# Kernel optimization log

Hardware: AMD Instinct MI355X
Metric: run time of the kernel (lower is better)

The kernel has to match this reference:

```python
import jax, jax.numpy as jnp
import numpy as np

B, T, D, H = 2, 2048, 1024, 16
DH = D // H
PD = 6
SCALE = DH ** -0.5
_PAIRS4 = [(0, 1), (0, 2), (0, 3), (1, 2), (1, 3), (2, 3)]
_J6 = jnp.array([[0, 0, 0, 0, 0, 1], [0, 0, 0, 0, -1, 0], [0, 0, 0, 1, 0, 0],
                 [0, 0, 1, 0, 0, 0], [0, -1, 0, 0, 0, 0], [1, 0, 0, 0, 0, 0]], dtype=jnp.float32)


def exterior(p1, p2):
    # p1, p2: (..., 4) -> normalized 6-d Plucker line (..., 6)
    parts = [p1[..., i] * p2[..., j] - p1[..., j] * p2[..., i] for i, j in _PAIRS4]
    L = jnp.stack(parts, axis=-1)
    n = jnp.linalg.norm(L, axis=-1, keepdims=True)
    return L / jnp.clip(n, 1e-12)


def setup_inputs() -> dict:
    key = jax.random.key(0)
    ks = jax.random.split(key, 12)
    s = 0.02
    return {
        'x': jax.random.normal(ks[0], (B, T, D), jnp.float32),
        'qkv_w': jax.random.normal(ks[1], (D, 3 * D), jnp.float32) * s,
        'qkv_b': jnp.zeros((3 * D,), jnp.float32),
        'w1_write': jax.random.normal(ks[2], (D, 4 * H), jnp.float32) * s,
        'w2_write': jax.random.normal(ks[3], (D, 4 * H), jnp.float32) * s,
        'w1_read': jax.random.normal(ks[4], (D, 4 * H), jnp.float32) * s,
        'w2_read': jax.random.normal(ks[5], (D, 4 * H), jnp.float32) * s,
        'memv_w': jax.random.normal(ks[6], (D, D), jnp.float32) * s,
        'memv_b': jnp.zeros((D,), jnp.float32),
        'memg_w': jax.random.normal(ks[7], (D, H), jnp.float32) * s,
        'memg_b': jnp.zeros((H,), jnp.float32),
        'mem_scale': jnp.full((H,), 0.1, jnp.float32),
        'rw_mix': jnp.zeros((), jnp.float32),
        'out_w': jax.random.normal(ks[8], (D, D), jnp.float32) * s,
        'out_b': jnp.zeros((D,), jnp.float32),
        'decay_logits': jnp.full((H,), 4.6, jnp.float32),
    }


def reference(x, qkv_w, qkv_b, w1_write, w2_write, w1_read, w2_read,
              memv_w, memv_b, memg_w, memg_b, mem_scale, rw_mix,
              out_w, out_b, decay_logits):
    # ---- standard causal softmax attention ----
    qkv = (x @ qkv_w + qkv_b).reshape(B, T, 3, H, DH).transpose(2, 0, 3, 1, 4)
    q, k, v = qkv[0], qkv[1], qkv[2]                      # each (B,H,T,DH)
    scores = jnp.einsum('bhtd,bhsd->bhts', q, k) * SCALE
    mask = jnp.triu(jnp.ones((T, T), bool), 1)
    scores = jnp.where(mask[None, None], -jnp.inf, scores)
    attn = jax.nn.softmax(scores, axis=-1)                # dropout=0 (eval)
    seq_out = jnp.einsum('bhts,bhsd->bthd', attn, v).reshape(B, T, D)

    # ---- Plucker lines for write (prev->cur) and read ----
    x_prev = jnp.concatenate([jnp.zeros((B, 1, D), x.dtype), x[:, :-1]], axis=1)
    w1 = (x_prev @ w1_write).reshape(B, T, H, 4)
    w2 = (x @ w2_write).reshape(B, T, H, 4)
    write_lines = exterior(w1, w2)                        # (B,T,H,6)
    r1 = (x @ w1_read).reshape(B, T, H, 4)
    r2 = (x @ w2_read).reshape(B, T, H, 4)
    read_lines = exterior(r1, r2)

    Jw = jnp.einsum('bthi,ij->bhtj', write_lines, _J6)    # (B,H,T,6)
    Jr = jnp.einsum('bthi,ij->bhtj', read_lines, _J6)
    rd = read_lines.transpose(0, 2, 1, 3)                 # (B,H,T,6)

    # ---- decay-weighted cumsum of 6x6 outer-product states ----
    decays = jax.nn.sigmoid(decay_logits)                 # (H,)
    pos = jnp.arange(T, dtype=x.dtype)
    decay_inv = (1.0 / jnp.clip(decays, 1e-6))[:, None] ** pos[None]   # (H,T)
    decay_fwd = decays[:, None] ** pos[None]                           # (H,T)

    def shifted_state(Jv):
        outer = Jv[..., :, None] * Jv[..., None, :]       # (B,H,T,6,6)
        ow = outer * decay_inv[None, :, :, None, None]
        M = jnp.cumsum(ow, axis=2)
        M = jnp.concatenate([jnp.zeros((B, H, 1, PD, PD), x.dtype), M[:, :, :-1]], axis=2)
        return M * decay_fwd[None, :, :, None, None]

    Mw = shifted_state(Jw)
    Mr = shifted_state(Jr)

    score_w = jnp.einsum('bhti,bhtij,bhtj->bht', rd, Mw, rd)
    score_r = jnp.einsum('bhti,bhtij,bhtj->bht', Jw, Mr, Jw)
    alpha = jax.nn.sigmoid(rw_mix)
    mem_score = (1 - alpha) * score_w + alpha * score_r   # (B,H,T)

    mem_val = x @ memv_w + memv_b                         # (B,T,D)
    gate = jax.nn.sigmoid(x @ memg_w + memg_b)            # (B,T,H)
    mem_score_t = mem_score.transpose(0, 2, 1)            # (B,T,H)
    gated = jax.nn.sigmoid(mem_score_t * mem_scale[None, None, :]) * gate
    gated = gated.mean(axis=-1, keepdims=True)            # (B,T,1)

    return (seq_out + gated * mem_val) @ out_w + out_b
```

## Files before the change

### kernel.cpp

```cpp
#include <hip/hip_runtime.h>

#define Bb 2
#define Tt 2048
#define Dd 1024
#define Hh 16
#define LDC 4480

typedef __attribute__((ext_vector_type(8))) short s16x8;
typedef __attribute__((ext_vector_type(4))) float f32x4;
typedef __attribute__((ext_vector_type(8))) _Float16 f16x8;

__device__ __forceinline__ float bf2f(unsigned short u) {
  unsigned v = ((unsigned)u) << 16;
  union { unsigned u; float f; } c; c.u = v; return c.f;
}
__device__ __forceinline__ unsigned short f2bf(float f) {
  union { float f; unsigned u; } c; c.f = f;
  unsigned u = c.u + 0x7fffu + ((c.u >> 16) & 1u);
  return (unsigned short)(u >> 16);
}
__device__ __forceinline__ float sigm(float x) { return 1.f / (1.f + expf(-x)); }

typedef const __attribute__((address_space(1))) void* gas_ptr;
typedef __attribute__((address_space(3))) void* las_ptr;
__device__ __forceinline__ void gload_lds16(const unsigned short* g, unsigned short* l) {
  __builtin_amdgcn_global_load_lds((gas_ptr)g, (las_ptr)l, 16, 0, 0);
}



__global__ __launch_bounds__(256) void prep_kernel(const float* __restrict__ x,
                                                   const float* __restrict__ qkv_w,
                                                   const float* __restrict__ w1w,
                                                   const float* __restrict__ w2w,
                                                   const float* __restrict__ w1r,
                                                   const float* __restrict__ w2r,
                                                   const float* __restrict__ memg_w,
                                                   const float* __restrict__ memv_w,
                                                   const float* __restrict__ out_w,
                                                   const float* __restrict__ qkv_b,
                                                   const float* __restrict__ memg_b,
                                                   const float* __restrict__ memv_b,
                                                   unsigned short* __restrict__ xb,
                                                   unsigned short* __restrict__ WT,
                                                   unsigned short* __restrict__ outT,
                                                   float* __restrict__ biasC) {
  __shared__ float tile[32][33];
  int id = blockIdx.x;
  if (id < 2048) {
    int i = id * 256 + threadIdx.x;
    int row = i >> 7;
    int k8 = i & 127;
    const float4* xv = reinterpret_cast<const float4*>(x + (size_t)i * 8);
    float4 a = xv[0], b = xv[1];
    s16x8 out;
    out[0] = (short)f2bf(a.x); out[1] = (short)f2bf(a.y);
    out[2] = (short)f2bf(a.z); out[3] = (short)f2bf(a.w);
    out[4] = (short)f2bf(b.x); out[5] = (short)f2bf(b.y);
    out[6] = (short)f2bf(b.z); out[7] = (short)f2bf(b.w);
    int mt = row >> 4, kt = k8 >> 2, quad = k8 & 3;
    int lane = (row & 15) + quad * 16;
    *(s16x8*)&xb[(((size_t)mt * 32 + kt) * 64 + lane) * 8] = out;
  } else if (id < 6528) {
    int j = id - 2048;
    int n0 = (j % 140) * 32, kt = j / 140, k0 = kt * 32;
    int tx = threadIdx.x & 31, ty = threadIdx.x >> 5;
#pragma unroll
    for (int i = 0; i < 4; i++) {
      int k = k0 + ty + i * 8, n = n0 + tx;
      float v;
      if (n < 3072)       v = qkv_w[(size_t)k * 3072 + n];
      else if (n < 3136)  v = w1w[k * 64 + (n - 3072)];
      else if (n < 3200)  v = w2w[k * 64 + (n - 3136)];
      else if (n < 3264)  v = w1r[k * 64 + (n - 3200)];
      else if (n < 3328)  v = w2r[k * 64 + (n - 3264)];
      else if (n < 3344)  v = memg_w[k * 16 + (n - 3328)];
      else if (n < 3392)  v = 0.f;
      else if (n < 4416)  v = memv_w[(size_t)k * 1024 + (n - 3392)];
      else                v = 0.f;
      tile[ty + i * 8][tx] = v;
    }
    __syncthreads();
    if (threadIdx.x < 128) {
      int nl = threadIdx.x & 31, quad = threadIdx.x >> 5;
      s16x8 out;
#pragma unroll
      for (int e = 0; e < 8; e++) out[e] = (short)f2bf(tile[quad * 8 + e][nl]);
      int nt = (n0 >> 4) + (nl >> 4);
      int lane = (nl & 15) + quad * 16;
      *(s16x8*)&WT[(((size_t)nt * 32 + kt) * 64 + lane) * 8] = out;
    }
  } else if (id < 7552) {
    int j = id - 6528;
    int n0 = (j & 31) * 32, kt = j >> 5, k0 = kt * 32;
    int tx = threadIdx.x & 31, ty = threadIdx.x >> 5;
#pragma unroll
    for (int i = 0; i < 4; i++) {
      int k = k0 + ty + i * 8, n = n0 + tx;
      tile[ty + i * 8][tx] = out_w[(size_t)k * 1024 + n];
    }
    __syncthreads();
    if (threadIdx.x < 128) {
      int nl = threadIdx.x & 31, quad = threadIdx.x >> 5;
      s16x8 out;
#pragma unroll
      for (int e = 0; e < 8; e++) out[e] = (short)f2bf(tile[quad * 8 + e][nl]);
      int nt = (n0 >> 4) + (nl >> 4);
      int lane = (nl & 15) + quad * 16;
      *(s16x8*)&outT[(((size_t)nt * 32 + kt) * 64 + lane) * 8] = out;
    }
  } else {
    int i = (id - 7552) * 256 + threadIdx.x;
    if (i < LDC) {
      float v = 0.f;
      if (i < 3072) v = qkv_b[i];
      else if (i >= 3328 && i < 3344) v = memg_b[i - 3328];
      else if (i >= 3392 && i < 4416) v = memv_b[i - 3392];
      biasC[i] = v;
    }
  }
}


__global__ __launch_bounds__(256, 2) void gemm_fat_kernel(const unsigned short* __restrict__ Af,
                                                          const unsigned short* __restrict__ Bf,
                                                          unsigned short* __restrict__ Cout,
                                                          const float* __restrict__ bias) {
  const int blk = blockIdx.x;
  const int xcd = blk & 7, local = blk >> 3;
  const int mTile = (xcd & 3) * 8 + (local & 7);
  const int nTile = (xcd >> 2) * 9 + (local >> 3);
  const int lane = threadIdx.x & 63, wid = threadIdx.x >> 6;
  const int quad = lane >> 4, c16 = lane & 15;
  const int wm = wid & 1, wn = wid >> 1;
  const int mt0 = mTile * 8 + wm * 4;
  const int nt0 = nTile * 16 + wn * 8;

  const unsigned short* Apt = Af + ((size_t)mt0 * 32 * 64 + lane) * 8;
  const unsigned short* Bpt = Bf + ((size_t)nt0 * 32 * 64 + lane) * 8;

  f32x4 acc[4][8] = {};
  s16x8 af[2][4];
  s16x8 bf[2][8];
#pragma unroll
  for (int i = 0; i < 4; i++) af[0][i] = *(const s16x8*)(Apt + (size_t)i * 16384);
#pragma unroll
  for (int j = 0; j < 8; j++) bf[0][j] = *(const s16x8*)(Bpt + (size_t)j * 16384);

#pragma unroll
  for (int kt = 0; kt < 32; kt++) {
    const int cur = kt & 1, nxt = cur ^ 1;
    if (kt + 1 < 32) {
      const unsigned short* An = Apt + (size_t)(kt + 1) * 512;
      const unsigned short* Bn = Bpt + (size_t)(kt + 1) * 512;
#pragma unroll
      for (int i = 0; i < 4; i++) af[nxt][i] = *(const s16x8*)(An + (size_t)i * 16384);
#pragma unroll
      for (int j = 0; j < 8; j++) bf[nxt][j] = *(const s16x8*)(Bn + (size_t)j * 16384);
    }
#pragma unroll
    for (int i = 0; i < 4; i++)
#pragma unroll
      for (int j = 0; j < 8; j++)
        acc[i][j] = __builtin_amdgcn_mfma_f32_16x16x32_bf16(af[cur][i], bf[cur][j],
                                                            acc[i][j], 0, 0, 0);
  }

#pragma unroll
  for (int i = 0; i < 4; i++)
#pragma unroll
    for (int j = 0; j < 8; j++) {
      if (nt0 + j < 280) {
        int col = (nt0 + j) * 16 + c16;
        float bv = bias[col];
#pragma unroll
        for (int r = 0; r < 4; r++) {
          int row = (mt0 + i) * 16 + quad * 4 + r;
          Cout[(size_t)row * 4480 + col] = f2bf(acc[i][j][r] + bv);
        }
      }
    }
}


template <int MODE>
__global__ __launch_bounds__(256) void gemm_frag_kernel(const unsigned short* __restrict__ Af,
                                                        const unsigned short* __restrict__ Bf,
                                                        void* __restrict__ Cout,
                                                        const float* __restrict__ bias) {
  __shared__ __align__(16) unsigned short lds[2][16][512];
  int mTile, nTile;
  if (MODE == 0) {
    const int xx = blockIdx.x & 7, local = blockIdx.x >> 3;
    mTile = (xx >> 1) * 8 + (local & 7);
    nTile = (xx & 1) * 18 + (local >> 3);
    if (nTile >= 35) return;
  } else {
    mTile = blockIdx.x >> 3;
    nTile = blockIdx.x & 7;
  }
  const int lane = threadIdx.x & 63, wid = threadIdx.x >> 6;
  const int quad = lane >> 4, c16 = lane & 15;
  const int wm = wid >> 1, wn = wid & 1;
  const int mt0 = mTile * 8 + wm * 4;
  const int nt0 = nTile * 8 + wn * 4;

  const unsigned short* src[4];
#pragma unroll
  for (int i = 0; i < 4; i++) {
    int f = wid * 4 + i;
    src[i] = ((f < 8) ? (Af + (size_t)(mTile * 8 + f) * 16384)
                      : (Bf + (size_t)(nTile * 8 + (f - 8)) * 16384))
             + (size_t)lane * 8;
  }

  f32x4 acc[4][4] = {};

#pragma unroll
  for (int i = 0; i < 4; i++) gload_lds16(src[i], &lds[0][wid * 4 + i][0]);
  __syncthreads();

  int buf = 0;
  for (int kt = 0; kt < 32; kt++) {
    if (kt + 1 < 32) {
#pragma unroll
      for (int i = 0; i < 4; i++)
        gload_lds16(src[i] + (size_t)(kt + 1) * 512, &lds[buf ^ 1][wid * 4 + i][0]);
    }
    s16x8 a[4], b[4];
#pragma unroll
    for (int i = 0; i < 4; i++) {
      a[i] = *(const s16x8*)&lds[buf][wm * 4 + i][lane * 8];
      b[i] = *(const s16x8*)&lds[buf][8 + wn * 4 + i][lane * 8];
    }
#pragma unroll
    for (int mt = 0; mt < 4; mt++)
#pragma unroll
      for (int nt = 0; nt < 4; nt++)
        acc[mt][nt] = __builtin_amdgcn_mfma_f32_16x16x32_bf16(a[mt], b[nt],
                                                              acc[mt][nt], 0, 0, 0);
    __syncthreads();
    buf ^= 1;
  }

#pragma unroll
  for (int mt = 0; mt < 4; mt++)
#pragma unroll
    for (int nt = 0; nt < 4; nt++) {
      int col = (nt0 + nt) * 16 + c16;
      float bv = bias[col];
#pragma unroll
      for (int r = 0; r < 4; r++) {
        int row = (mt0 + mt) * 16 + quad * 4 + r;
        if (MODE == 0)
          ((unsigned short*)Cout)[(size_t)row * 4480 + col] = f2bf(acc[mt][nt][r] + bv);
        else
          ((float*)Cout)[(size_t)row * 1024 + col] = acc[mt][nt][r] + bv;
      }
    }
}


__device__ __forceinline__ void ext6(const float* p, const float* q, float* L) {
  L[0] = p[0] * q[1] - p[1] * q[0];
  L[1] = p[0] * q[2] - p[2] * q[0];
  L[2] = p[0] * q[3] - p[3] * q[0];
  L[3] = p[1] * q[2] - p[2] * q[1];
  L[4] = p[1] * q[3] - p[3] * q[1];
  L[5] = p[2] * q[3] - p[3] * q[2];
  float n = sqrtf(L[0]*L[0] + L[1]*L[1] + L[2]*L[2] + L[3]*L[3] + L[4]*L[4] + L[5]*L[5]);
  float inv = 1.f / fmaxf(n, 1e-12f);
#pragma unroll
  for (int k = 0; k < 6; k++) L[k] *= inv;
}


__global__ __launch_bounds__(256) void post1_kernel(const unsigned short* __restrict__ Cq,
                                                    unsigned short* __restrict__ Kt,
                                                    unsigned short* __restrict__ Vt,
                                                    float* __restrict__ Jw,
                                                    float* __restrict__ Jr,
                                                    float* __restrict__ rd) {
  __shared__ unsigned short vt[32 * 66];
  int id = blockIdx.x;
  int tid = threadIdx.x;
  if (id < 2048) {
    int kb = id & 63, bh = id >> 6;
    int b = bh >> 4, h = bh & 15;
    size_t tbase = ((size_t)bh * 64 + kb) * 2048;
    {
      int key = tid >> 3, p = tid & 7, dg = p ^ (key & 7);
      size_t src = (size_t)(b * Tt + kb * 32 + key) * LDC + 1024 + h * 64 + dg * 8;
      s16x8 kv = *(const s16x8*)&Cq[src];
      s16x8 kvs;
#pragma unroll
      for (int e = 0; e < 8; e++)
        kvs[e] = (short)f2bf(bf2f((unsigned short)kv[e]) * 0.125f);
      *(s16x8*)&Kt[tbase + (size_t)tid * 8] = kvs;
    }
    {
      int row = tid >> 3, c = tid & 7;
      size_t src = (size_t)(b * Tt + kb * 32 + row) * LDC + 2048 + h * 64 + c * 8;
      s16x8 vv = *(const s16x8*)&Cq[src];
#pragma unroll
      for (int e = 0; e < 8; e++) {
        union { _Float16 hf; unsigned short s; } cv;
        cv.hf = (_Float16)bf2f((unsigned short)vv[e]);
        vt[row * 66 + c * 8 + e] = cv.s;
      }
    }
    __syncthreads();
    {
      int d = tid >> 2, p = tid & 3, cq = p ^ ((d >> 2) & 3);
      s16x8 out;
#pragma unroll
      for (int e = 0; e < 8; e++) {
        int key = ((e >> 2) & 1) * 16 + cq * 4 + (e & 3);
        out[e] = (short)vt[key * 66 + d];
      }
      *(s16x8*)&Vt[tbase + (size_t)tid * 8] = out;
    }
  } else {
    int idx = (id - 2048) * 256 + tid;
    int h = idx & 15, t = (idx >> 4) & 2047, b = idx >> 15;
    size_t row = (size_t)(b * Tt + t) * LDC;
    float w1[4], w2[4], r1[4], r2[4];
#pragma unroll
    for (int k = 0; k < 4; k++) {
      w1[k] = (t > 0) ? bf2f(Cq[row - LDC + 3072 + h * 4 + k]) : 0.f;
      w2[k] = bf2f(Cq[row + 3136 + h * 4 + k]);
      r1[k] = bf2f(Cq[row + 3200 + h * 4 + k]);
      r2[k] = bf2f(Cq[row + 3264 + h * 4 + k]);
    }
    float Lw[6], Lr[6];
    ext6(w1, w2, Lw);
    ext6(r1, r2, Lr);
    size_t ob = ((size_t)(b * Hh + h) * Tt + t) * 6;
    Jw[ob + 0] = Lw[5]; Jw[ob + 1] = -Lw[4]; Jw[ob + 2] = Lw[3];
    Jw[ob + 3] = Lw[2]; Jw[ob + 4] = -Lw[1]; Jw[ob + 5] = Lw[0];
    Jr[ob + 0] = Lr[5]; Jr[ob + 1] = -Lr[4]; Jr[ob + 2] = Lr[3];
    Jr[ob + 3] = Lr[2]; Jr[ob + 4] = -Lr[1]; Jr[ob + 5] = Lr[0];
#pragma unroll
    for (int k = 0; k < 6; k++) rd[ob + k] = Lr[k];
  }
}


__device__ __forceinline__ void do_tile(int ks, int q0, int quad, int c16,
                                        const s16x8& qf0, const s16x8& qf1,
                                        const s16x8 kf[2][2], const f16x8 vb[4],
                                        float& l_i, f32x4 o[4]) {
  f32x4 st0 = {}, st1 = {};
  __builtin_amdgcn_s_setprio(1);
  st0 = __builtin_amdgcn_mfma_f32_16x16x32_bf16(kf[0][0], qf0, st0, 0, 0, 0);
  st0 = __builtin_amdgcn_mfma_f32_16x16x32_bf16(kf[0][1], qf1, st0, 0, 0, 0);
  st1 = __builtin_amdgcn_mfma_f32_16x16x32_bf16(kf[1][0], qf0, st1, 0, 0, 0);
  st1 = __builtin_amdgcn_mfma_f32_16x16x32_bf16(kf[1][1], qf1, st1, 0, 0, 0);
  __builtin_amdgcn_s_setprio(0);
  bool need_mask = (ks + 31 > q0);
  f16x8 pa;
  float lp = 0.f;
#pragma unroll
  for (int r = 0; r < 4; r++) {
    float v0 = st0[r];
    float v1 = st1[r];
    if (need_mask) {
      v0 = (ks + quad * 4 + r      <= q0 + c16) ? v0 : -1e30f;
      v1 = (ks + 16 + quad * 4 + r <= q0 + c16) ? v1 : -1e30f;
    }
    float p0 = __expf(v0);
    float p1 = __expf(v1);
    lp += p0 + p1;
    pa[r]     = (_Float16)p0;
    pa[4 + r] = (_Float16)p1;
  }
  l_i += lp;
  __builtin_amdgcn_s_setprio(1);
#pragma unroll
  for (int nt = 0; nt < 4; nt++)
    o[nt] = __builtin_amdgcn_mfma_f32_16x16x32_f16(pa, vb[nt], o[nt], 0, 0, 0);
  __builtin_amdgcn_s_setprio(0);
}

__global__ __launch_bounds__(128, 2) void attn_kernel(const unsigned short* __restrict__ Cq,
                                                      const unsigned short* __restrict__ Kt,
                                                      const unsigned short* __restrict__ Vt,
                                                      unsigned short* __restrict__ po) {
  __shared__ float mrg[64][69];
  const int id = blockIdx.x;
  const int xcd = id & 7, rest = id >> 3;
  const int j = rest & 31;
  const int bh = ((rest >> 5) << 3) | xcd;
  const int b = bh >> 4, h = bh & 15;
  const int kw = threadIdx.x >> 6, lane = threadIdx.x & 63;
  const int quad = lane >> 4, c16 = lane & 15;
  const int qA0r = j * 32,        qA1r = j * 32 + 16;
  const int qB0r = 2016 - j * 32, qB1r = 2032 - j * 32;
  const int Ttot = 64 - j;
  const int ht = (j >= 16) ? 16 : (32 - j);
  const int t0 = kw ? ht : 0;
  const int t1 = kw ? Ttot : ht;
  const char* Kbase = (const char*)(Kt + (size_t)bh * 64 * 2048);
  const char* Vbase = (const char*)(Vt + (size_t)bh * 64 * 2048);
  const int vK0 = c16 * 128 + ((quad       ^ (c16 & 7)) * 16);
  const int vK1 = c16 * 128 + (((4 + quad) ^ (c16 & 7)) * 16);
  const int vV  = c16 * 64  + ((quad ^ ((c16 >> 2) & 3)) * 16);

  size_t rowA0 = (size_t)(b * Tt + qA0r + c16) * LDC + h * 64;
  size_t rowA1 = (size_t)(b * Tt + qA1r + c16) * LDC + h * 64;
  size_t rowB0 = (size_t)(b * Tt + qB0r + c16) * LDC + h * 64;
  size_t rowB1 = (size_t)(b * Tt + qB1r + c16) * LDC + h * 64;
  s16x8 qa00 = *(const s16x8*)&Cq[rowA0 + quad * 8];
  s16x8 qa01 = *(const s16x8*)&Cq[rowA0 + 32 + quad * 8];
  s16x8 qa10 = *(const s16x8*)&Cq[rowA1 + quad * 8];
  s16x8 qa11 = *(const s16x8*)&Cq[rowA1 + 32 + quad * 8];
  s16x8 qb00 = *(const s16x8*)&Cq[rowB0 + quad * 8];
  s16x8 qb01 = *(const s16x8*)&Cq[rowB0 + 32 + quad * 8];
  s16x8 qb10 = *(const s16x8*)&Cq[rowB1 + quad * 8];
  s16x8 qb11 = *(const s16x8*)&Cq[rowB1 + 32 + quad * 8];

  float lA0 = 0.f, lA1 = 0.f, lB0 = 0.f, lB1 = 0.f;
  f32x4 oA0[4] = {}, oA1[4] = {}, oB0[4] = {}, oB1[4] = {};

  s16x8 kfX[2][2], kfY[2][2];
  f16x8 vbX[4], vbY[4];

#define LOADT(dstK, dstV, kb) do {                                   \
    const char* Kb_ = Kbase + (size_t)(kb) * 4096;                   \
    const char* Vb_ = Vbase + (size_t)(kb) * 4096;                   \
    dstK[0][0] = *(const s16x8*)(Kb_ + vK0);                         \
    dstK[0][1] = *(const s16x8*)(Kb_ + vK1);                         \
    dstK[1][0] = *(const s16x8*)(Kb_ + 2048 + vK0);                  \
    dstK[1][1] = *(const s16x8*)(Kb_ + 2048 + vK1);                  \
    dstV[0] = *(const f16x8*)(Vb_ + vV);                             \
    dstV[1] = *(const f16x8*)(Vb_ + 1024 + vV);                      \
    dstV[2] = *(const f16x8*)(Vb_ + 2048 + vV);                      \
    dstV[3] = *(const f16x8*)(Vb_ + 3072 + vV);                      \
  } while (0)

#define DOTILES(KF, VF, t) do {                                      \
    int ks_ = (t) * 32;                                              \
    do_tile(ks_, qB0r, quad, c16, qb00, qb01, KF, VF, lB0, oB0);     \
    do_tile(ks_, qB1r, quad, c16, qb10, qb11, KF, VF, lB1, oB1);     \
    if ((t) <= j) {                                                  \
      do_tile(ks_, qA0r, quad, c16, qa00, qa01, KF, VF, lA0, oA0);   \
      do_tile(ks_, qA1r, quad, c16, qa10, qa11, KF, VF, lA1, oA1);   \
    }                                                                \
  } while (0)

  LOADT(kfX, vbX, t0);
  for (int t = t0; t < t1; t += 2) {
    if (t + 1 < t1) LOADT(kfY, vbY, t + 1);
    DOTILES(kfX, vbX, t);
    if (t + 1 < t1) {
      if (t + 2 < t1) LOADT(kfX, vbX, t + 2);
      DOTILES(kfY, vbY, t + 1);
    }
  }
#undef DOTILES
#undef LOADT

  if (kw == 1) {
#pragma unroll
    for (int nt = 0; nt < 4; nt++)
#pragma unroll
      for (int r = 0; r < 4; r++) {
        mrg[lane][nt * 4 + r]      = oB0[nt][r];
        mrg[lane][16 + nt * 4 + r] = oB1[nt][r];
        mrg[lane][32 + nt * 4 + r] = oA0[nt][r];
        mrg[lane][48 + nt * 4 + r] = oA1[nt][r];
      }
    mrg[lane][64] = lB0;
    mrg[lane][65] = lB1;
    mrg[lane][66] = lA0;
    mrg[lane][67] = lA1;
  }
  __syncthreads();
  if (kw == 1) return;
#pragma unroll
  for (int nt = 0; nt < 4; nt++)
#pragma unroll
    for (int r = 0; r < 4; r++) {
      oB0[nt][r] += mrg[lane][nt * 4 + r];
      oB1[nt][r] += mrg[lane][16 + nt * 4 + r];
      oA0[nt][r] += mrg[lane][32 + nt * 4 + r];
      oA1[nt][r] += mrg[lane][48 + nt * 4 + r];
    }
  lB0 += mrg[lane][64];
  lB1 += mrg[lane][65];
  lA0 += mrg[lane][66];
  lA1 += mrg[lane][67];

  lB0 += __shfl_xor(lB0, 16, 64); lB0 += __shfl_xor(lB0, 32, 64);
  lB1 += __shfl_xor(lB1, 16, 64); lB1 += __shfl_xor(lB1, 32, 64);
  lA0 += __shfl_xor(lA0, 16, 64); lA0 += __shfl_xor(lA0, 32, 64);
  lA1 += __shfl_xor(lA1, 16, 64); lA1 += __shfl_xor(lA1, 32, 64);
  float invB0 = 1.f / lB0, invB1 = 1.f / lB1;
  float invA0 = 1.f / lA0, invA1 = 1.f / lA1;
#pragma unroll
  for (int r = 0; r < 4; r++) {
    float ivB0 = __shfl(invB0, quad * 4 + r, 64);
    float ivB1 = __shfl(invB1, quad * 4 + r, 64);
    float ivA0 = __shfl(invA0, quad * 4 + r, 64);
    float ivA1 = __shfl(invA1, quad * 4 + r, 64);
    size_t bB0 = (size_t)(b * Tt + qB0r + quad * 4 + r) * Dd + h * 64;
    size_t bB1 = (size_t)(b * Tt + qB1r + quad * 4 + r) * Dd + h * 64;
    size_t bA0 = (size_t)(b * Tt + qA0r + quad * 4 + r) * Dd + h * 64;
    size_t bA1 = (size_t)(b * Tt + qA1r + quad * 4 + r) * Dd + h * 64;
#pragma unroll
    for (int nt = 0; nt < 4; nt++) {
      po[bB0 + nt * 16 + c16] = f2bf(oB0[nt][r] * ivB0);
      po[bB1 + nt * 16 + c16] = f2bf(oB1[nt][r] * ivB1);
      po[bA0 + nt * 16 + c16] = f2bf(oA0[nt][r] * ivA0);
      po[bA1 + nt * 16 + c16] = f2bf(oA1[nt][r] * ivA1);
    }
  }
}


__global__ __launch_bounds__(64) void scanA_kernel(const float* __restrict__ Jw,
                                                   const float* __restrict__ Jr,
                                                   const float* __restrict__ decay_logits,
                                                   float* __restrict__ chunkA) {
  int blk = blockIdx.x;
  int chunk = blk & 15, bh = (blk >> 4) & 31, type = blk >> 9;
  int lane = threadIdx.x;
  const float* V = (type == 0 ? Jw : Jr) + ((size_t)bh * Tt + chunk * 128) * 6;
  __shared__ float v[768];
  for (int i = lane; i < 768; i += 64) v[i] = V[i];
  __syncthreads();
  float d = sigm(decay_logits[bh & 15]);
  int ll = lane < 36 ? lane : 35;
  int i6 = ll / 6, j6 = ll % 6;
  float A = 0.f;
  for (int s = 0; s < 128; s++) A = d * A + v[s * 6 + i6] * v[s * 6 + j6];
  if (lane < 36) chunkA[((size_t)(type * 32 + bh) * 16 + chunk) * 36 + lane] = A;
}


__global__ __launch_bounds__(128) void scanB_kernel(const float* __restrict__ Jw,
                                                    const float* __restrict__ Jr,
                                                    const float* __restrict__ rd,
                                                    const float* __restrict__ chunkA,
                                                    const float* __restrict__ decay_logits,
                                                    float* __restrict__ score_w,
                                                    float* __restrict__ score_r) {
  int blk = blockIdx.x;
  int chunk = blk & 15, bh = (blk >> 4) & 31, type = blk >> 9;
  int tl = threadIdx.x;
  size_t tb = ((size_t)bh * Tt + chunk * 128) * 6;
  const float* U = (type == 0 ? rd : Jw) + tb;
  const float* W = (type == 0 ? Jw : Jr) + tb;
  __shared__ float wv[768];
  __shared__ float Bm[36];
  for (int i = tl; i < 768; i += 128) wv[i] = W[i];
  float d = sigm(decay_logits[bh & 15]);
  if (tl < 36) {
    float dS = powf(d, 128.f);
    float Bv = 0.f;
    size_t base = (size_t)(type * 32 + bh) * 16;
    for (int c = 0; c < chunk; c++)
      Bv = dS * Bv + d * chunkA[(base + c) * 36 + tl];
    Bm[tl] = Bv;
  }
  __syncthreads();
  float u[6];
#pragma unroll
  for (int i = 0; i < 6; i++) u[i] = U[tl * 6 + i];
  float q = 0.f;
#pragma unroll
  for (int i = 0; i < 6; i++) {
    float bi = 0.f;
#pragma unroll
    for (int j = 0; j < 6; j++) bi += Bm[i * 6 + j] * u[j];
    q += u[i] * bi;
  }
  float acc = 0.f;
  for (int s = 0; s < tl; s++) {
    const float* ws = &wv[s * 6];
    float dot = u[0]*ws[0] + u[1]*ws[1] + u[2]*ws[2] + u[3]*ws[3] + u[4]*ws[4] + u[5]*ws[5];
    acc = d * (acc + dot * dot);
  }
  float score = acc + powf(d, (float)tl) * q;
  float* outp = (type == 0 ? score_w : score_r);
  outp[(size_t)bh * Tt + chunk * 128 + tl] = score;
}


__global__ __launch_bounds__(256) void combine_kernel(const unsigned short* __restrict__ po,
                                                      const unsigned short* __restrict__ Cq,
                                                      const float* __restrict__ score_w,
                                                      const float* __restrict__ score_r,
                                                      const float* __restrict__ mem_scale,
                                                      const float* __restrict__ rw_mix,
                                                      unsigned short* __restrict__ fused) {
  __shared__ float tmp[16];
  int rowi = blockIdx.x;
  int b = rowi >> 11, t = rowi & 2047;
  float alpha = sigm(rw_mix[0]);
  if (threadIdx.x < 16) {
    int h = threadIdx.x;
    size_t sh = (size_t)(b * 16 + h) * Tt + t;
    float ms = (1.f - alpha) * score_w[sh] + alpha * score_r[sh];
    float gate = sigm(bf2f(Cq[(size_t)rowi * LDC + 3328 + h]));
    tmp[h] = sigm(ms * mem_scale[h]) * gate;
  }
  __syncthreads();
  float g = 0.f;
#pragma unroll
  for (int h = 0; h < 16; h++) g += tmp[h];
  g *= (1.f / 16.f);
  if (threadIdx.x < 128) {
    int c = threadIdx.x;
    int d0 = c * 8;
    s16x8 ov = *(const s16x8*)&po[((size_t)b * Tt + t) * Dd + d0];
    s16x8 mv = *(const s16x8*)&Cq[(size_t)rowi * LDC + 3392 + d0];
    s16x8 out;
#pragma unroll
    for (int e = 0; e < 8; e++)
      out[e] = (short)f2bf(bf2f((unsigned short)ov[e]) + g * bf2f((unsigned short)mv[e]));
    int mt = rowi >> 4, kt = c >> 2, quad = c & 3;
    int lane = (rowi & 15) + quad * 16;
    *(s16x8*)&fused[(((size_t)mt * 32 + kt) * 64 + lane) * 8] = out;
  }
}


extern "C" void kernel_launch(void* const* d_in, const int* in_sizes, int n_in,
                              void* d_out, int out_size, void* d_ws, size_t ws_size,
                              hipStream_t stream) {
  (void)in_sizes; (void)n_in; (void)out_size; (void)ws_size;
  const float* x         = (const float*)d_in[0];
  const float* qkv_w     = (const float*)d_in[1];
  const float* qkv_b     = (const float*)d_in[2];
  const float* w1w       = (const float*)d_in[3];
  const float* w2w       = (const float*)d_in[4];
  const float* w1r       = (const float*)d_in[5];
  const float* w2r       = (const float*)d_in[6];
  const float* memv_w    = (const float*)d_in[7];
  const float* memv_b    = (const float*)d_in[8];
  const float* memg_w    = (const float*)d_in[9];
  const float* memg_b    = (const float*)d_in[10];
  const float* mem_scale = (const float*)d_in[11];
  const float* rw_mix    = (const float*)d_in[12];
  const float* out_w     = (const float*)d_in[13];
  const float* out_b     = (const float*)d_in[14];
  const float* decay_l   = (const float*)d_in[15];

  char* w = (char*)d_ws;
  unsigned short* xb    = (unsigned short*)(w + 0);
  unsigned short* Kt    = (unsigned short*)(w + 0);
  unsigned short* WT    = (unsigned short*)(w + 8388608);
  unsigned short* Vt    = (unsigned short*)(w + 8388608);
  unsigned short* outT  = (unsigned short*)(w + 17563648);
  float*          biasC = (float*)(w + 19660800);
  unsigned short* Cbuf  = (unsigned short*)(w + 19678720);
  unsigned short* po    = (unsigned short*)(w + 56378880);
  float*          Jw    = (float*)(w + 73680384);
  float*          Jr    = (float*)(w + 75253248);
  float*          rd    = (float*)(w + 76826112);
  float*          chA   = (float*)(w + 78398976);
  float*          sw    = (float*)(w + 78693888);
  float*          sr    = (float*)(w + 78956032);
  unsigned short* fused = (unsigned short*)(w + 79218176);

  prep_kernel<<<7570, 256, 0, stream>>>(x, qkv_w, w1w, w2w, w1r, w2r, memg_w, memv_w,
                                        out_w, qkv_b, memg_b, memv_b,
                                        xb, WT, outT, biasC);

  gemm_fat_kernel<<<576, 256, 0, stream>>>(xb, WT, Cbuf, biasC);

  post1_kernel<<<2304, 256, 0, stream>>>(Cbuf, Kt, Vt, Jw, Jr, rd);
  attn_kernel<<<1024, 128, 0, stream>>>(Cbuf, Kt, Vt, po);
  scanA_kernel<<<1024, 64, 0, stream>>>(Jw, Jr, decay_l, chA);
  scanB_kernel<<<1024, 128, 0, stream>>>(Jw, Jr, rd, chA, decay_l, sw, sr);
  combine_kernel<<<4096, 256, 0, stream>>>(po, Cbuf, sw, sr, mem_scale, rw_mix, fused);

  gemm_frag_kernel<1><<<256, 256, 0, stream>>>(fused, outT, d_out, out_b);
}
```

Baseline: 305.4 us.

## Rebalance prep, QKV GEMM, combine and output GEMM grids

The weight-transpose prep blocks now each handle four k-tiles, which cuts the prep grid to fewer blocks. The register-fed fat QKV GEMM is replaced by the LDS-staged frag GEMM in mode 0. The combine kernel now processes two rows per block so all 256 threads do work. A new output GEMM with 128x64 tiles launches 512 blocks instead of 256 for better CU occupancy. Each change trades per-block work against launch overhead and parallelism, and the swapped QKV GEMM path may behave differently in performance.

```diff
diff --git a/kernel.cpp b/kernel.cpp
--- a/kernel.cpp
+++ b/kernel.cpp
@@ -61,56 +61,64 @@
     int mt = row >> 4, kt = k8 >> 2, quad = k8 & 3;
     int lane = (row & 15) + quad * 16;
     *(s16x8*)&xb[(((size_t)mt * 32 + kt) * 64 + lane) * 8] = out;
-  } else if (id < 6528) {
+  } else if (id < 3168) {
     int j = id - 2048;
-    int n0 = (j % 140) * 32, kt = j / 140, k0 = kt * 32;
+    int n0 = (j % 140) * 32, kt0 = (j / 140) * 4;
     int tx = threadIdx.x & 31, ty = threadIdx.x >> 5;
-#pragma unroll
-    for (int i = 0; i < 4; i++) {
-      int k = k0 + ty + i * 8, n = n0 + tx;
-      float v;
-      if (n < 3072)       v = qkv_w[(size_t)k * 3072 + n];
-      else if (n < 3136)  v = w1w[k * 64 + (n - 3072)];
-      else if (n < 3200)  v = w2w[k * 64 + (n - 3136)];
-      else if (n < 3264)  v = w1r[k * 64 + (n - 3200)];
-      else if (n < 3328)  v = w2r[k * 64 + (n - 3264)];
-      else if (n < 3344)  v = memg_w[k * 16 + (n - 3328)];
-      else if (n < 3392)  v = 0.f;
-      else if (n < 4416)  v = memv_w[(size_t)k * 1024 + (n - 3392)];
-      else                v = 0.f;
-      tile[ty + i * 8][tx] = v;
-    }
-    __syncthreads();
-    if (threadIdx.x < 128) {
-      int nl = threadIdx.x & 31, quad = threadIdx.x >> 5;
-      s16x8 out;
-#pragma unroll
-      for (int e = 0; e < 8; e++) out[e] = (short)f2bf(tile[quad * 8 + e][nl]);
-      int nt = (n0 >> 4) + (nl >> 4);
-      int lane = (nl & 15) + quad * 16;
-      *(s16x8*)&WT[(((size_t)nt * 32 + kt) * 64 + lane) * 8] = out;
-    }
-  } else if (id < 7552) {
-    int j = id - 6528;
-    int n0 = (j & 31) * 32, kt = j >> 5, k0 = kt * 32;
+    for (int kk = 0; kk < 4; kk++) {
+      int kt = kt0 + kk, k0 = kt * 32;
+#pragma unroll
+      for (int i = 0; i < 4; i++) {
+        int k = k0 + ty + i * 8, n = n0 + tx;
+        float v;
+        if (n < 3072)       v = qkv_w[(size_t)k * 3072 + n];
+        else if (n < 3136)  v = w1w[k * 64 + (n - 3072)];
+        else if (n < 3200)  v = w2w[k * 64 + (n - 3136)];
+        else if (n < 3264)  v = w1r[k * 64 + (n - 3200)];
+        else if (n < 3328)  v = w2r[k * 64 + (n - 3264)];
+        else if (n < 3344)  v = memg_w[k * 16 + (n - 3328)];
+        else if (n < 3392)  v = 0.f;
+        else if (n < 4416)  v = memv_w[(size_t)k * 1024 + (n - 3392)];
+        else                v = 0.f;
+        tile[ty + i * 8][tx] = v;
+      }
+      __syncthreads();
+      if (threadIdx.x < 128) {
+        int nl = threadIdx.x & 31, quad = threadIdx.x >> 5;
+        s16x8 out;
+#pragma unroll
+        for (int e = 0; e < 8; e++) out[e] = (short)f2bf(tile[quad * 8 + e][nl]);
+        int nt = (n0 >> 4) + (nl >> 4);
+        int lane = (nl & 15) + quad * 16;
+        *(s16x8*)&WT[(((size_t)nt * 32 + kt) * 64 + lane) * 8] = out;
+      }
+      __syncthreads();
+    }
+  } else if (id < 3424) {
+    int j = id - 3168;
+    int n0 = (j & 31) * 32, kt0 = (j >> 5) * 4;
     int tx = threadIdx.x & 31, ty = threadIdx.x >> 5;
-#pragma unroll
-    for (int i = 0; i < 4; i++) {
-      int k = k0 + ty + i * 8, n = n0 + tx;
-      tile[ty + i * 8][tx] = out_w[(size_t)k * 1024 + n];
-    }
-    __syncthreads();
-    if (threadIdx.x < 128) {
-      int nl = threadIdx.x & 31, quad = threadIdx.x >> 5;
-      s16x8 out;
-#pragma unroll
-      for (int e = 0; e < 8; e++) out[e] = (short)f2bf(tile[quad * 8 + e][nl]);
-      int nt = (n0 >> 4) + (nl >> 4);
-      int lane = (nl & 15) + quad * 16;
-      *(s16x8*)&outT[(((size_t)nt * 32 + kt) * 64 + lane) * 8] = out;
+    for (int kk = 0; kk < 4; kk++) {
+      int kt = kt0 + kk, k0 = kt * 32;
+#pragma unroll
+      for (int i = 0; i < 4; i++) {
+        int k = k0 + ty + i * 8, n = n0 + tx;
+        tile[ty + i * 8][tx] = out_w[(size_t)k * 1024 + n];
+      }
+      __syncthreads();
+      if (threadIdx.x < 128) {
+        int nl = threadIdx.x & 31, quad = threadIdx.x >> 5;
+        s16x8 out;
+#pragma unroll
+        for (int e = 0; e < 8; e++) out[e] = (short)f2bf(tile[quad * 8 + e][nl]);
+        int nt = (n0 >> 4) + (nl >> 4);
+        int lane = (nl & 15) + quad * 16;
+        *(s16x8*)&outT[(((size_t)nt * 32 + kt) * 64 + lane) * 8] = out;
+      }
+      __syncthreads();
     }
   } else {
-    int i = (id - 7552) * 256 + threadIdx.x;
+    int i = (id - 3424) * 256 + threadIdx.x;
     if (i < LDC) {
       float v = 0.f;
       if (i < 3072) v = qkv_b[i];
@@ -119,67 +127,6 @@
       biasC[i] = v;
     }
   }
-}
-
-
-__global__ __launch_bounds__(256, 2) void gemm_fat_kernel(const unsigned short* __restrict__ Af,
-                                                          const unsigned short* __restrict__ Bf,
-                                                          unsigned short* __restrict__ Cout,
-                                                          const float* __restrict__ bias) {
-  const int blk = blockIdx.x;
-  const int xcd = blk & 7, local = blk >> 3;
-  const int mTile = (xcd & 3) * 8 + (local & 7);
-  const int nTile = (xcd >> 2) * 9 + (local >> 3);
-  const int lane = threadIdx.x & 63, wid = threadIdx.x >> 6;
-  const int quad = lane >> 4, c16 = lane & 15;
-  const int wm = wid & 1, wn = wid >> 1;
-  const int mt0 = mTile * 8 + wm * 4;
-  const int nt0 = nTile * 16 + wn * 8;
-
-  const unsigned short* Apt = Af + ((size_t)mt0 * 32 * 64 + lane) * 8;
-  const unsigned short* Bpt = Bf + ((size_t)nt0 * 32 * 64 + lane) * 8;
-
-  f32x4 acc[4][8] = {};
-  s16x8 af[2][4];
-  s16x8 bf[2][8];
-#pragma unroll
-  for (int i = 0; i < 4; i++) af[0][i] = *(const s16x8*)(Apt + (size_t)i * 16384);
-#pragma unroll
-  for (int j = 0; j < 8; j++) bf[0][j] = *(const s16x8*)(Bpt + (size_t)j * 16384);
-
-#pragma unroll
-  for (int kt = 0; kt < 32; kt++) {
-    const int cur = kt & 1, nxt = cur ^ 1;
-    if (kt + 1 < 32) {
-      const unsigned short* An = Apt + (size_t)(kt + 1) * 512;
-      const unsigned short* Bn = Bpt + (size_t)(kt + 1) * 512;
-#pragma unroll
-      for (int i = 0; i < 4; i++) af[nxt][i] = *(const s16x8*)(An + (size_t)i * 16384);
-#pragma unroll
-      for (int j = 0; j < 8; j++) bf[nxt][j] = *(const s16x8*)(Bn + (size_t)j * 16384);
-    }
-#pragma unroll
-    for (int i = 0; i < 4; i++)
-#pragma unroll
-      for (int j = 0; j < 8; j++)
-        acc[i][j] = __builtin_amdgcn_mfma_f32_16x16x32_bf16(af[cur][i], bf[cur][j],
-                                                            acc[i][j], 0, 0, 0);
-  }
-
-#pragma unroll
-  for (int i = 0; i < 4; i++)
-#pragma unroll
-    for (int j = 0; j < 8; j++) {
-      if (nt0 + j < 280) {
-        int col = (nt0 + j) * 16 + c16;
-        float bv = bias[col];
-#pragma unroll
-        for (int r = 0; r < 4; r++) {
-          int row = (mt0 + i) * 16 + quad * 4 + r;
-          Cout[(size_t)row * 4480 + col] = f2bf(acc[i][j][r] + bv);
-        }
-      }
-    }
 }
 
 
@@ -256,6 +203,73 @@
           ((unsigned short*)Cout)[(size_t)row * 4480 + col] = f2bf(acc[mt][nt][r] + bv);
         else
           ((float*)Cout)[(size_t)row * 1024 + col] = acc[mt][nt][r] + bv;
+      }
+    }
+}
+
+
+__global__ __launch_bounds__(256) void gemm_out_kernel(const unsigned short* __restrict__ Af,
+                                                       const unsigned short* __restrict__ Bf,
+                                                       float* __restrict__ Cout,
+                                                       const float* __restrict__ bias) {
+  __shared__ __align__(16) unsigned short lds[2][12][512];
+  const int mTile = blockIdx.x >> 4;
+  const int nTile = blockIdx.x & 15;
+  const int lane = threadIdx.x & 63, wid = threadIdx.x >> 6;
+  const int quad = lane >> 4, c16 = lane & 15;
+  const int wm = wid >> 1, wn = wid & 1;
+  const int mt0 = mTile * 8 + wm * 4;
+  const int nt0 = nTile * 4 + wn * 2;
+
+  const unsigned short* src[3];
+#pragma unroll
+  for (int i = 0; i < 3; i++) {
+    int f = wid * 3 + i;
+    src[i] = ((f < 8) ? (Af + (size_t)(mTile * 8 + f) * 16384)
+                      : (Bf + (size_t)(nTile * 4 + (f - 8)) * 16384))
+             + (size_t)lane * 8;
+  }
+
+  f32x4 acc[4][2] = {};
+
+#pragma unroll
+  for (int i = 0; i < 3; i++) gload_lds16(src[i], &lds[0][wid * 3 + i][0]);
+  __syncthreads();
+
+  int buf = 0;
+  for (int kt = 0; kt < 32; kt++) {
+    if (kt + 1 < 32) {
+#pragma unroll
+      for (int i = 0; i < 3; i++)
+        gload_lds16(src[i] + (size_t)(kt + 1) * 512, &lds[buf ^ 1][wid * 3 + i][0]);
+    }
+    s16x8 a[4], b[2];
+#pragma unroll
+    for (int i = 0; i < 4; i++)
+      a[i] = *(const s16x8*)&lds[buf][wm * 4 + i][lane * 8];
+#pragma unroll
+    for (int j = 0; j < 2; j++)
+      b[j] = *(const s16x8*)&lds[buf][8 + wn * 2 + j][lane * 8];
+#pragma unroll
+    for (int i = 0; i < 4; i++)
+#pragma unroll
+      for (int j = 0; j < 2; j++)
+        acc[i][j] = __builtin_amdgcn_mfma_f32_16x16x32_bf16(a[i], b[j],
+                                                            acc[i][j], 0, 0, 0);
+    __syncthreads();
+    buf ^= 1;
+  }
+
+#pragma unroll
+  for (int i = 0; i < 4; i++)
+#pragma unroll
+    for (int j = 0; j < 2; j++) {
+      int col = (nt0 + j) * 16 + c16;
+      float bv = bias[col];
+#pragma unroll
+      for (int r = 0; r < 4; r++) {
+        int row = (mt0 + i) * 16 + quad * 4 + r;
+        Cout[(size_t)row * 1024 + col] = acc[i][j][r] + bv;
       }
     }
 }
@@ -594,24 +608,26 @@
                                                       const float* __restrict__ mem_scale,
                                                       const float* __restrict__ rw_mix,
                                                       unsigned short* __restrict__ fused) {
-  __shared__ float tmp[16];
-  int rowi = blockIdx.x;
+  __shared__ float tmp[2][16];
+  int half = threadIdx.x >> 7;
+  int tid = threadIdx.x & 127;
+  int rowi = blockIdx.x * 2 + half;
   int b = rowi >> 11, t = rowi & 2047;
   float alpha = sigm(rw_mix[0]);
-  if (threadIdx.x < 16) {
-    int h = threadIdx.x;
+  if (tid < 16) {
+    int h = tid;
     size_t sh = (size_t)(b * 16 + h) * Tt + t;
     float ms = (1.f - alpha) * score_w[sh] + alpha * score_r[sh];
     float gate = sigm(bf2f(Cq[(size_t)rowi * LDC + 3328 + h]));
-    tmp[h] = sigm(ms * mem_scale[h]) * gate;
+    tmp[half][h] = sigm(ms * mem_scale[h]) * gate;
   }
   __syncthreads();
   float g = 0.f;
 #pragma unroll
-  for (int h = 0; h < 16; h++) g += tmp[h];
+  for (int h = 0; h < 16; h++) g += tmp[half][h];
   g *= (1.f / 16.f);
-  if (threadIdx.x < 128) {
-    int c = threadIdx.x;
+  {
+    int c = tid;
     int d0 = c * 8;
     s16x8 ov = *(const s16x8*)&po[((size_t)b * Tt + t) * Dd + d0];
     s16x8 mv = *(const s16x8*)&Cq[(size_t)rowi * LDC + 3392 + d0];
@@ -664,17 +680,17 @@
   float*          sr    = (float*)(w + 78956032);
   unsigned short* fused = (unsigned short*)(w + 79218176);
 
-  prep_kernel<<<7570, 256, 0, stream>>>(x, qkv_w, w1w, w2w, w1r, w2r, memg_w, memv_w,
+  prep_kernel<<<3442, 256, 0, stream>>>(x, qkv_w, w1w, w2w, w1r, w2r, memg_w, memv_w,
                                         out_w, qkv_b, memg_b, memv_b,
                                         xb, WT, outT, biasC);
 
-  gemm_fat_kernel<<<576, 256, 0, stream>>>(xb, WT, Cbuf, biasC);
+  gemm_frag_kernel<0><<<1152, 256, 0, stream>>>(xb, WT, Cbuf, biasC);
 
   post1_kernel<<<2304, 256, 0, stream>>>(Cbuf, Kt, Vt, Jw, Jr, rd);
   attn_kernel<<<1024, 128, 0, stream>>>(Cbuf, Kt, Vt, po);
   scanA_kernel<<<1024, 64, 0, stream>>>(Jw, Jr, decay_l, chA);
   scanB_kernel<<<1024, 128, 0, stream>>>(Jw, Jr, rd, chA, decay_l, sw, sr);
-  combine_kernel<<<4096, 256, 0, stream>>>(po, Cbuf, sw, sr, mem_scale, rw_mix, fused);
-
-  gemm_frag_kernel<1><<<256, 256, 0, stream>>>(fused, outT, d_out, out_b);
-}
+  combine_kernel<<<2048, 256, 0, stream>>>(po, Cbuf, sw, sr, mem_scale, rw_mix, fused);
+
+  gemm_out_kernel<<<512, 256, 0, stream>>>(fused, outT, (float*)d_out, out_b);
+}
```

New measurement: 250.8 us. -17.9%, faster.
